# Optimization experiments

Measured on AMD Instinct MI355X. Metric: run time of the kernel, lower is better.

Reference implementation:

```python
import jax, jax.numpy as jnp
import numpy as np

NUM_EXPERTS = 16
HIDDEN_DIM = 1024
TOP_K = 4
INPUT_DIM = 4096
OUTPUT_DIM = 4096
BATCH = 4096


def setup_inputs() -> dict:
    key = jax.random.key(0)
    ks = jax.random.split(key, 6)
    total_cols = NUM_EXPERTS * HIDDEN_DIM
    return {
        "x": jax.random.normal(ks[0], (BATCH, INPUT_DIM), dtype=jnp.float32),
        "gate_w": jax.random.normal(ks[1], (INPUT_DIM, NUM_EXPERTS), dtype=jnp.float32) * 0.02,
        "gate_b": jnp.zeros((NUM_EXPERTS,), dtype=jnp.float32),
        "weight": jax.random.normal(ks[2], (INPUT_DIM, total_cols), dtype=jnp.float32) * 0.01,
        "agg_w": jax.random.normal(ks[3], (total_cols, OUTPUT_DIM), dtype=jnp.float32) * 0.02,
        "agg_b": jnp.zeros((OUTPUT_DIM,), dtype=jnp.float32),
    }


def reference(x, gate_w, gate_b, weight, agg_w, agg_b):
    # 1) gating logits (batch, E), 2) sum over batch -> (E,)
    gating_logits = x @ gate_w + gate_b
    gating_sum = gating_logits.sum(axis=0)
    # 3) global top-k expert selection -> binary mask over experts
    _, topk_inds = jax.lax.top_k(gating_sum, TOP_K)
    expert_mask = jnp.zeros((NUM_EXPERTS,), dtype=x.dtype).at[topk_inds].set(1.0)
    # 4/5) block-sparse matmul: mask replicated over all row blocks, so each
    # expert's column block [e*H:(e+1)*H] is x @ W_block if selected else 0.
    out_sparse = x @ weight  # (batch, E*H)
    col_mask = jnp.repeat(expert_mask, HIDDEN_DIM)  # (E*H,)
    out_sparse = out_sparse * col_mask[None, :]
    # 6) aggregator
    final_out = out_sparse @ agg_w + agg_b
    return final_out
```

## Files before the change

kernel.cpp:

```cpp
#include <hip/hip_runtime.h>
#include <hip/hip_bf16.h>


#define BATCH 4096
#define DIN 4096
#define DOUTD 4096
#define NE 16
#define HD 1024
#define TOPK 4
#define TOTC (NE * HD)

using bf16 = __hip_bfloat16;
typedef __attribute__((ext_vector_type(8))) short short8;
typedef __attribute__((ext_vector_type(4))) float f32x4;

__device__ inline short f2bs(float f) {
  __hip_bfloat16 h = __float2bfloat16(f);
  return *reinterpret_cast<short*>(&h);
}

__global__ void k_pcol(const float* __restrict__ x, float* __restrict__ pcol) {
  int c = blockIdx.x * 256 + threadIdx.x;
  int r0 = blockIdx.y * 128;
  float s = 0.f;
  for (int r = r0; r < r0 + 128; ++r) s += x[(size_t)r * DIN + c];
  pcol[(size_t)blockIdx.y * DIN + c] = s;
}

__global__ void k_red(const float* __restrict__ pcol, float* __restrict__ colsum) {
  int c = blockIdx.x * 256 + threadIdx.x;
  float s = 0.f;
  for (int j = 0; j < 32; ++j) s += pcol[(size_t)j * DIN + c];
  colsum[c] = s;
}

__global__ void k_gate(const float* __restrict__ colsum, const float* __restrict__ gw,
                       const float* __restrict__ gb, int* __restrict__ ids) {
  __shared__ float red[4][16];
  __shared__ float gs[16];
  int t = threadIdx.x;
  int e = t & 15, kg = t >> 4;
  float p = 0.f;
  for (int k = kg; k < DIN; k += 16) p += colsum[k] * gw[(size_t)k * NE + e];
  p += __shfl_down(p, 32);
  p += __shfl_down(p, 16);
  if ((t & 63) < 16) red[t >> 6][e] = p;
  __syncthreads();
  if (t < 16) gs[t] = red[0][t] + red[1][t] + red[2][t] + red[3][t] + (float)BATCH * gb[t];
  __syncthreads();
  if (t == 0) {
    float v[16];
    #pragma unroll
    for (int i = 0; i < 16; ++i) v[i] = gs[i];
    for (int j = 0; j < TOPK; ++j) {
      int bi = 0;
      float bv = v[0];
      for (int i2 = 1; i2 < 16; ++i2) {
        if (v[i2] > bv) { bv = v[i2]; bi = i2; }
      }
      ids[j] = bi;
      v[bi] = -3.4e38f;
    }
  }
}

__global__ void k_cvt_x(const float* __restrict__ x, bf16* __restrict__ xb) {
  size_t i = ((size_t)blockIdx.x * 256 + threadIdx.x) * 8;
  float4 v0 = *reinterpret_cast<const float4*>(x + i);
  float4 v1 = *reinterpret_cast<const float4*>(x + i + 4);
  short8 r;
  r[0] = f2bs(v0.x); r[1] = f2bs(v0.y); r[2] = f2bs(v0.z); r[3] = f2bs(v0.w);
  r[4] = f2bs(v1.x); r[5] = f2bs(v1.y); r[6] = f2bs(v1.z); r[7] = f2bs(v1.w);
  *reinterpret_cast<short8*>(reinterpret_cast<char*>(xb) + i * 2) = r;
}

__global__ void k_gather_w(const float* __restrict__ w, const int* __restrict__ ids,
                           bf16* __restrict__ wbt) {
  __shared__ float tile[32][33];
  int bid = blockIdx.x;
  int k0 = (bid & 127) * 32, n0 = (bid >> 7) * 32;
  int t = threadIdx.x;
  int tx = t & 31, ty = t >> 5;
  int e = ids[n0 >> 10];
  size_t wcol = (size_t)e * HD + (n0 & 1023) + tx;
  #pragma unroll
  for (int j = 0; j < 4; ++j) {
    int k = k0 + ty + j * 8;
    tile[ty + j * 8][tx] = w[(size_t)k * TOTC + wcol];
  }
  __syncthreads();
  #pragma unroll
  for (int j = 0; j < 4; ++j) {
    int n = n0 + ty + j * 8;
    wbt[(size_t)n * DIN + k0 + tx] = __float2bfloat16(tile[tx][ty + j * 8]);
  }
}

__global__ void k_gather_a(const float* __restrict__ a, const int* __restrict__ ids,
                           bf16* __restrict__ abt) {
  __shared__ float tile[32][33];
  int bid = blockIdx.x;
  int k0 = (bid & 127) * 32, n0 = (bid >> 7) * 32;
  int t = threadIdx.x;
  int tx = t & 31, ty = t >> 5;
  int e = ids[k0 >> 10];
  #pragma unroll
  for (int j = 0; j < 4; ++j) {
    int k = k0 + ty + j * 8;
    size_t ar = (size_t)e * HD + (k & 1023);
    tile[ty + j * 8][tx] = a[ar * DOUTD + n0 + tx];
  }
  __syncthreads();
  #pragma unroll
  for (int j = 0; j < 4; ++j) {
    int n = n0 + ty + j * 8;
    abt[(size_t)n * DIN + k0 + tx] = __float2bfloat16(tile[tx][ty + j * 8]);
  }
}

template <int STORE_F32>
__global__ __launch_bounds__(256, 2) void k_gemm(
    const bf16* __restrict__ A, const bf16* __restrict__ Bt,
    bf16* __restrict__ Cb, float* __restrict__ Cf, const float* __restrict__ bias) {
  __shared__ char smraw[65536];
  const int t = threadIdx.x;
  const int lane = t & 63;
  const int w = t >> 6;
  const int bm = blockIdx.y * 128, bn = blockIdx.x * 128;
  const int wr = (w >> 1) * 64, wc = (w & 1) * 64;

  f32x4 acc[4][4] = {};

  const int sr = t >> 3;
  const int sc = t & 7;
  const int scs = (sc ^ (sr & 7)) * 8;

  auto STAGE = [&](int buf, int kt) {
    char* lbase = smraw + buf * 32768;
    #pragma unroll
    for (int i = 0; i < 4; ++i) {
      const bf16* ga = A + (size_t)(bm + i * 32 + sr) * 4096 + kt * 64 + scs;
      __builtin_amdgcn_global_load_lds(
          (const __attribute__((address_space(1))) void*)ga,
          (__attribute__((address_space(3))) void*)(lbase + i * 4096 + t * 16), 16, 0, 0);
    }
    #pragma unroll
    for (int i = 0; i < 4; ++i) {
      const bf16* gb = Bt + (size_t)(bn + i * 32 + sr) * 4096 + kt * 64 + scs;
      __builtin_amdgcn_global_load_lds(
          (const __attribute__((address_space(1))) void*)gb,
          (__attribute__((address_space(3))) void*)(lbase + 16384 + i * 4096 + t * 16), 16, 0, 0);
    }
  };

  auto COMPUTE = [&](int buf) {
    const char* sa = smraw + buf * 32768;
    const char* sb = sa + 16384;
    #pragma unroll
    for (int kk = 0; kk < 2; ++kk) {
      short8 af[4], bfr[4];
      #pragma unroll
      for (int m = 0; m < 4; ++m) {
        int row = wr + m * 16 + (lane & 15);
        int kb = (kk * 64 + ((lane >> 4) * 16)) ^ ((row & 7) * 16);
        af[m] = *reinterpret_cast<const short8*>(sa + row * 128 + kb);
      }
      #pragma unroll
      for (int n = 0; n < 4; ++n) {
        int row = wc + n * 16 + (lane & 15);
        int kb = (kk * 64 + ((lane >> 4) * 16)) ^ ((row & 7) * 16);
        bfr[n] = *reinterpret_cast<const short8*>(sb + row * 128 + kb);
      }
      #pragma unroll
      for (int m = 0; m < 4; ++m)
        #pragma unroll
        for (int n = 0; n < 4; ++n)
          acc[m][n] = __builtin_amdgcn_mfma_f32_16x16x32_bf16(af[m], bfr[n], acc[m][n], 0, 0, 0);
    }
  };

  STAGE(0, 0);
  asm volatile("s_waitcnt vmcnt(0)" ::: "memory");
  __syncthreads();
  int cur = 0;
  for (int kt = 0; kt < 63; ++kt) {
    STAGE(cur ^ 1, kt + 1);
    COMPUTE(cur);
    asm volatile("s_waitcnt vmcnt(0)" ::: "memory");
    __syncthreads();
    cur ^= 1;
  }
  COMPUTE(cur);

  const int cr = (lane >> 4) * 4;
  const int cc = lane & 15;
  #pragma unroll
  for (int m = 0; m < 4; ++m) {
    #pragma unroll
    for (int n = 0; n < 4; ++n) {
      int row = bm + wr + m * 16 + cr;
      int col = bn + wc + n * 16 + cc;
      #pragma unroll
      for (int r = 0; r < 4; ++r) {
        if constexpr (STORE_F32) {
          Cf[(size_t)(row + r) * 4096 + col] = acc[m][n][r] + bias[col];
        } else {
          Cb[(size_t)(row + r) * 4096 + col] = __float2bfloat16(acc[m][n][r]);
        }
      }
    }
  }
}

extern "C" void kernel_launch(void* const* d_in, const int* in_sizes, int n_in,
                              void* d_out, int out_size, void* d_ws, size_t ws_size,
                              hipStream_t stream) {
  const float* x = (const float*)d_in[0];
  const float* gate_w = (const float*)d_in[1];
  const float* gate_b = (const float*)d_in[2];
  const float* weight = (const float*)d_in[3];
  const float* agg_w = (const float*)d_in[4];
  const float* agg_b = (const float*)d_in[5];
  float* out = (float*)d_out;
  char* ws = (char*)d_ws;

  float* pcol = (float*)ws;
  float* colsum = (float*)(ws + 524288);
  int* ids = (int*)(ws + 540672);
  bf16* mid = (bf16*)(ws + (1u << 20));
  bf16* abt = (bf16*)(ws + (1u << 20) + (32u << 20));
  bf16* xb = (bf16*)d_out;
  bf16* wbt = (bf16*)((char*)d_out + (32u << 20));

  k_pcol<<<dim3(16, 32), 256, 0, stream>>>(x, pcol);
  k_red<<<16, 256, 0, stream>>>(pcol, colsum);
  k_gate<<<1, 256, 0, stream>>>(colsum, gate_w, gate_b, ids);
  k_cvt_x<<<8192, 256, 0, stream>>>(x, xb);
  k_gather_w<<<16384, 256, 0, stream>>>(weight, ids, wbt);
  k_gemm<0><<<dim3(32, 32), 256, 0, stream>>>(xb, wbt, mid, nullptr, nullptr);
  k_gather_a<<<16384, 256, 0, stream>>>(agg_w, ids, abt);
  k_gemm<1><<<dim3(32, 32), 256, 0, stream>>>(mid, abt, nullptr, out, agg_b);
}
```

Measured before the change: 447.0 us.

## Replace GEMM with 256x256-tile 8-wave kernel using interleaved staged loads

Both bf16 GEMMs now use a 256x256 output tile per 512-thread block (8 waves, each computing 128x64) with 128KB of double-buffered LDS instead of 128x128 tiles. Global-to-LDS loads are split into quarter stages interleaved with MFMA clusters, separated by barriers and raised wave priority. A block-index swizzle groups tiles for L2 reuse. The larger tile halves global traffic per FLOP, at the cost of occupancy (256 blocks on 256 CUs) and more barrier synchronisation.

```diff
diff --git a/kernel.cpp b/kernel.cpp
--- a/kernel.cpp
+++ b/kernel.cpp
@@ -9,6 +9,7 @@
 #define HD 1024
 #define TOPK 4
 #define TOTC (NE * HD)
+#define NT 64
 
 using bf16 = __hip_bfloat16;
 typedef __attribute__((ext_vector_type(8))) short short8;
@@ -118,94 +119,140 @@
   }
 }
 
+#define MFMA_BF16 __builtin_amdgcn_mfma_f32_16x16x32_bf16
+
+#define MFMA16(MF0)                                                             \
+  __builtin_amdgcn_s_setprio(1);                                               \
+  _Pragma("unroll") for (int nf = 0; nf < 4; ++nf) {                            \
+    acc[MF0][nf] = MFMA_BF16(aA0, bfrag[nf][0], acc[MF0][nf], 0, 0, 0);         \
+    acc[MF0][nf] = MFMA_BF16(aA1, bfrag[nf][1], acc[MF0][nf], 0, 0, 0);         \
+    acc[MF0 + 1][nf] = MFMA_BF16(aB0, bfrag[nf][0], acc[MF0 + 1][nf], 0, 0, 0); \
+    acc[MF0 + 1][nf] = MFMA_BF16(aB1, bfrag[nf][1], acc[MF0 + 1][nf], 0, 0, 0); \
+  }                                                                             \
+  __builtin_amdgcn_s_setprio(0);
+
 template <int STORE_F32>
-__global__ __launch_bounds__(256, 2) void k_gemm(
+__global__ __launch_bounds__(512, 2) void k_gemm8(
     const bf16* __restrict__ A, const bf16* __restrict__ Bt,
     bf16* __restrict__ Cb, float* __restrict__ Cf, const float* __restrict__ bias) {
-  __shared__ char smraw[65536];
+  __shared__ __align__(16) char smraw[131072];
   const int t = threadIdx.x;
   const int lane = t & 63;
   const int w = t >> 6;
-  const int bm = blockIdx.y * 128, bn = blockIdx.x * 128;
-  const int wr = (w >> 1) * 64, wc = (w & 1) * 64;
-
-  f32x4 acc[4][4] = {};
-
-  const int sr = t >> 3;
-  const int sc = t & 7;
-  const int scs = (sc ^ (sr & 7)) * 8;
-
-  auto STAGE = [&](int buf, int kt) {
-    char* lbase = smraw + buf * 32768;
-    #pragma unroll
-    for (int i = 0; i < 4; ++i) {
-      const bf16* ga = A + (size_t)(bm + i * 32 + sr) * 4096 + kt * 64 + scs;
+  const int wr = w >> 2;
+  const int wc = w & 3;
+
+  const int bid = blockIdx.x;
+  const int swz = (bid & 7) * 32 + (bid >> 3);
+  const int bm = (swz >> 4) * 256;
+  const int bn = (swz & 15) * 256;
+
+  f32x4 acc[8][4] = {};
+  short8 bfrag[4][2];
+
+  const int srow = w * 16 + (lane >> 3);
+  const int sgr = lane & 7;
+
+  auto STAGE_A = [&](int buf, int half, int kt) {
+    char* lb = smraw + buf * 65536 + half * 16384 + w * 2048 + lane * 16;
+    #pragma unroll
+    for (int i = 0; i < 2; ++i) {
+      int r = srow + i * 8;
+      const bf16* g = A + (size_t)(bm + half * 128 + r) * 4096 + kt * 64 + ((sgr ^ (r & 7)) * 8);
       __builtin_amdgcn_global_load_lds(
-          (const __attribute__((address_space(1))) void*)ga,
-          (__attribute__((address_space(3))) void*)(lbase + i * 4096 + t * 16), 16, 0, 0);
-    }
-    #pragma unroll
-    for (int i = 0; i < 4; ++i) {
-      const bf16* gb = Bt + (size_t)(bn + i * 32 + sr) * 4096 + kt * 64 + scs;
+          (const __attribute__((address_space(1))) void*)g,
+          (__attribute__((address_space(3))) void*)(lb + i * 1024), 16, 0, 0);
+    }
+  };
+  auto STAGE_B = [&](int buf, int half, int kt) {
+    char* lb = smraw + buf * 65536 + 32768 + half * 16384 + w * 2048 + lane * 16;
+    #pragma unroll
+    for (int i = 0; i < 2; ++i) {
+      int r = srow + i * 8;
+      const bf16* g = Bt + (size_t)(bn + half * 128 + r) * 4096 + kt * 64 + ((sgr ^ (r & 7)) * 8);
       __builtin_amdgcn_global_load_lds(
-          (const __attribute__((address_space(1))) void*)gb,
-          (__attribute__((address_space(3))) void*)(lbase + 16384 + i * 4096 + t * 16), 16, 0, 0);
-    }
-  };
-
-  auto COMPUTE = [&](int buf) {
-    const char* sa = smraw + buf * 32768;
-    const char* sb = sa + 16384;
-    #pragma unroll
-    for (int kk = 0; kk < 2; ++kk) {
-      short8 af[4], bfr[4];
+          (const __attribute__((address_space(1))) void*)g,
+          (__attribute__((address_space(3))) void*)(lb + i * 1024), 16, 0, 0);
+    }
+  };
+  auto LDA = [&](int buf, int mf, int kk) -> short8 {
+    int r = mf * 16 + (lane & 15);
+    int kb = ((kk * 4 + (lane >> 4)) ^ (r & 7)) * 16;
+    return *reinterpret_cast<const short8*>(smraw + buf * 65536 + wr * 16384 + r * 128 + kb);
+  };
+  auto LDB = [&](int buf, int nf, int kk) -> short8 {
+    int nc = wc * 64 + nf * 16 + (lane & 15);
+    int half = nc >> 7, r = nc & 127;
+    int kb = ((kk * 4 + (lane >> 4)) ^ (r & 7)) * 16;
+    return *reinterpret_cast<const short8*>(smraw + buf * 65536 + 32768 + half * 16384 + r * 128 + kb);
+  };
+
+  STAGE_B(0, 0, 0); STAGE_B(0, 1, 0);
+  STAGE_A(0, 0, 0); STAGE_A(0, 1, 0);
+  STAGE_B(1, 0, 1); STAGE_B(1, 1, 1);
+  asm volatile("s_waitcnt vmcnt(4)" ::: "memory");
+  __builtin_amdgcn_s_barrier();
+
+  for (int j = 0; j < NT; ++j) {
+    const int cur = j & 1, nxt = cur ^ 1;
+    {
       #pragma unroll
-      for (int m = 0; m < 4; ++m) {
-        int row = wr + m * 16 + (lane & 15);
-        int kb = (kk * 64 + ((lane >> 4) * 16)) ^ ((row & 7) * 16);
-        af[m] = *reinterpret_cast<const short8*>(sa + row * 128 + kb);
-      }
-      #pragma unroll
-      for (int n = 0; n < 4; ++n) {
-        int row = wc + n * 16 + (lane & 15);
-        int kb = (kk * 64 + ((lane >> 4) * 16)) ^ ((row & 7) * 16);
-        bfr[n] = *reinterpret_cast<const short8*>(sb + row * 128 + kb);
-      }
-      #pragma unroll
-      for (int m = 0; m < 4; ++m)
-        #pragma unroll
-        for (int n = 0; n < 4; ++n)
-          acc[m][n] = __builtin_amdgcn_mfma_f32_16x16x32_bf16(af[m], bfr[n], acc[m][n], 0, 0, 0);
-    }
-  };
-
-  STAGE(0, 0);
-  asm volatile("s_waitcnt vmcnt(0)" ::: "memory");
-  __syncthreads();
-  int cur = 0;
-  for (int kt = 0; kt < 63; ++kt) {
-    STAGE(cur ^ 1, kt + 1);
-    COMPUTE(cur);
-    asm volatile("s_waitcnt vmcnt(0)" ::: "memory");
-    __syncthreads();
-    cur ^= 1;
-  }
-  COMPUTE(cur);
+      for (int nf = 0; nf < 4; ++nf) {
+        bfrag[nf][0] = LDB(cur, nf, 0);
+        bfrag[nf][1] = LDB(cur, nf, 1);
+      }
+      short8 aA0 = LDA(cur, 0, 0), aA1 = LDA(cur, 0, 1);
+      short8 aB0 = LDA(cur, 1, 0), aB1 = LDA(cur, 1, 1);
+      if (j + 1 < NT) STAGE_A(nxt, 0, j + 1);
+      __builtin_amdgcn_s_barrier();
+      MFMA16(0)
+      __builtin_amdgcn_s_barrier();
+    }
+    {
+      short8 aA0 = LDA(cur, 2, 0), aA1 = LDA(cur, 2, 1);
+      short8 aB0 = LDA(cur, 3, 0), aB1 = LDA(cur, 3, 1);
+      if (j + 1 < NT) STAGE_A(nxt, 1, j + 1);
+      __builtin_amdgcn_s_barrier();
+      MFMA16(2)
+      __builtin_amdgcn_s_barrier();
+    }
+    {
+      short8 aA0 = LDA(cur, 4, 0), aA1 = LDA(cur, 4, 1);
+      short8 aB0 = LDA(cur, 5, 0), aB1 = LDA(cur, 5, 1);
+      if (j + 2 < NT) STAGE_B(cur, 0, j + 2);
+      __builtin_amdgcn_s_barrier();
+      MFMA16(4)
+      __builtin_amdgcn_s_barrier();
+    }
+    {
+      short8 aA0 = LDA(cur, 6, 0), aA1 = LDA(cur, 6, 1);
+      short8 aB0 = LDA(cur, 7, 0), aB1 = LDA(cur, 7, 1);
+      if (j + 2 < NT) STAGE_B(cur, 1, j + 2);
+      if (j < NT - 2) {
+        asm volatile("s_waitcnt vmcnt(4)" ::: "memory");
+      } else {
+        asm volatile("s_waitcnt vmcnt(0)" ::: "memory");
+      }
+      __builtin_amdgcn_s_barrier();
+      MFMA16(6)
+      __builtin_amdgcn_s_barrier();
+    }
+  }
 
   const int cr = (lane >> 4) * 4;
   const int cc = lane & 15;
   #pragma unroll
-  for (int m = 0; m < 4; ++m) {
-    #pragma unroll
-    for (int n = 0; n < 4; ++n) {
-      int row = bm + wr + m * 16 + cr;
-      int col = bn + wc + n * 16 + cc;
+  for (int mf = 0; mf < 8; ++mf) {
+    #pragma unroll
+    for (int nf = 0; nf < 4; ++nf) {
+      int row = bm + wr * 128 + mf * 16 + cr;
+      int col = bn + wc * 64 + nf * 16 + cc;
       #pragma unroll
       for (int r = 0; r < 4; ++r) {
         if constexpr (STORE_F32) {
-          Cf[(size_t)(row + r) * 4096 + col] = acc[m][n][r] + bias[col];
+          Cf[(size_t)(row + r) * 4096 + col] = acc[mf][nf][r] + bias[col];
         } else {
-          Cb[(size_t)(row + r) * 4096 + col] = __float2bfloat16(acc[m][n][r]);
+          Cb[(size_t)(row + r) * 4096 + col] = __float2bfloat16(acc[mf][nf][r]);
         }
       }
     }
@@ -237,7 +284,7 @@
   k_gate<<<1, 256, 0, stream>>>(colsum, gate_w, gate_b, ids);
   k_cvt_x<<<8192, 256, 0, stream>>>(x, xb);
   k_gather_w<<<16384, 256, 0, stream>>>(weight, ids, wbt);
-  k_gemm<0><<<dim3(32, 32), 256, 0, stream>>>(xb, wbt, mid, nullptr, nullptr);
+  k_gemm8<0><<<256, 512, 0, stream>>>(xb, wbt, mid, nullptr, nullptr);
   k_gather_a<<<16384, 256, 0, stream>>>(agg_w, ids, abt);
-  k_gemm<1><<<dim3(32, 32), 256, 0, stream>>>(mid, abt, nullptr, out, agg_b);
-}
+  k_gemm8<1><<<256, 512, 0, stream>>>(mid, abt, nullptr, out, agg_b);
+}
```

New measurement: 410.6 us. 8.2% less time.
